# Kernel tuning notes

Hardware: AMD Instinct MI355X
Metric: run time of the kernel (lower is better)

Reference implementation:

```python
import jax, jax.numpy as jnp
import numpy as np

B, T, D_MODEL, HEAD_SIZE = 8, 1024, 1024, 64
BLOCK_SIZE = 1024  # == max_relative_pos


def setup_inputs() -> dict:
    key = jax.random.key(0)
    ks = jax.random.split(key, 7)
    s = 1.0 / np.sqrt(D_MODEL)
    return {
        "x": jax.random.normal(ks[0], (B, T, D_MODEL), dtype=jnp.float32),
        "Wk": jax.random.normal(ks[1], (D_MODEL, HEAD_SIZE), dtype=jnp.float32) * s,
        "bk": jax.random.normal(ks[2], (HEAD_SIZE,), dtype=jnp.float32) * 0.02,
        "Wq": jax.random.normal(ks[3], (D_MODEL, HEAD_SIZE), dtype=jnp.float32) * s,
        "bq": jax.random.normal(ks[4], (HEAD_SIZE,), dtype=jnp.float32) * 0.02,
        "Wv": jax.random.normal(ks[5], (D_MODEL, HEAD_SIZE), dtype=jnp.float32) * s,
        "rel_emb": jax.random.normal(ks[6], (2 * BLOCK_SIZE + 1, HEAD_SIZE), dtype=jnp.float32) * 0.02,
        "mask": 1,
    }


def reference(x, Wk, bk, Wq, bq, Wv, rel_emb, mask):
    Bb, Tt, _ = x.shape
    hs = Wk.shape[1]
    max_rel = (rel_emb.shape[0] - 1) // 2

    k = x @ Wk + bk          # [B,T,hs]
    q = x @ Wq + bq          # [B,T,hs]
    v = x @ Wv               # [B,T,hs]

    pos = jnp.arange(Tt)
    idx = jnp.clip(pos[:, None] - pos[None, :], -max_rel, max_rel) + max_rel
    r = rel_emb[idx]         # [T,T,hs], r[i,j] = emb(clip(i-j))

    # scores[b,i,j] = (q[b,i] + r[i,j]) . (k[b,j] + r[j,i]) / sqrt(hs)
    scale = 1.0 / np.sqrt(hs).astype(np.float32)
    scores = (
        jnp.einsum("bid,bjd->bij", q, k)
        + jnp.einsum("bid,jid->bij", q, r)   # q_i . r[j,i]
        + jnp.einsum("ijd,bjd->bij", r, k)   # r[i,j] . k_j
        + jnp.einsum("ijd,jid->ij", r, r)[None]  # r[i,j] . r[j,i]
    ) * scale

    if mask:  # static Python int -> causal mask, matches tril masked_fill
        causal = jnp.tril(jnp.ones((Tt, Tt), dtype=bool))
        scores = jnp.where(causal, scores, jnp.float32(-jnp.inf))

    w = jax.nn.softmax(scores, axis=-1)  # dropout is identity in eval mode
    return w @ v  # [B,T,hs]
```

## Files before the change

kernel.cpp:

```cpp
#include <hip/hip_runtime.h>
#include <hip/hip_bf16.h>
#include <math.h>


typedef __hip_bfloat16 bf16;
typedef __attribute__((ext_vector_type(8))) short short8;
typedef __attribute__((ext_vector_type(4))) float f32x4;

#define NTILE32 528
#define MFMA16(a, b, c) __builtin_amdgcn_mfma_f32_16x16x32_bf16(a, b, c, 0, 0, 0)

__device__ __forceinline__ float bf2f(bf16 h) { return __bfloat162float(h); }
__device__ __forceinline__ bf16 f2bf(float f) { return __float2bfloat16(f); }
__device__ __forceinline__ short bfs(float f) {
  bf16 h = __float2bfloat16(f);
  return *(short*)&h;
}

union U16 {
  uint4 u;
  short8 s;
};
__device__ __forceinline__ short8 ldfrag(const bf16* p) {
  U16 x;
  x.u = *(const uint4*)p;
  return x.s;
}

__global__ __launch_bounds__(256) void prep_kernel(
    const float* __restrict__ Wk, const float* __restrict__ Wq, const float* __restrict__ Wv,
    const float* __restrict__ E, bf16* __restrict__ WT, bf16* __restrict__ Ep,
    bf16* __restrict__ Erev, float* __restrict__ rrG, float* __restrict__ zeroBase) {
  const int bid = blockIdx.x, t = threadIdx.x;
  if (bid < 768) {
    int idx = bid * 256 + t;
    int sel = idx >> 16, r = idx & 65535;
    int n = r >> 10, kk = r & 1023;
    const float* W = (sel == 0) ? Wk : (sel == 1) ? Wq : Wv;
    WT[idx] = f2bf(W[kk * 64 + n]);
  } else if (bid < 1281) {
    int idx = (bid - 768) * 256 + t;
    if (idx < 2049 * 64) {
      int tt = idx >> 6, d = idx & 63;
      Ep[idx] = f2bf(E[idx]);
      Erev[idx] = f2bf(E[(size_t)(2048 - tt) * 64 + d]);
    }
  } else if (bid < 1537) {
    int dlt = ((bid - 1281) << 2) + (t >> 6);
    int d = t & 63;
    float p = E[(size_t)(1024 + dlt) * 64 + d] * E[(size_t)(1024 - dlt) * 64 + d];
#pragma unroll
    for (int off = 32; off > 0; off >>= 1) p += __shfl_down(p, off);
    if (d == 0) rrG[64 + dlt] = p;
  } else {
    int idx4 = (bid - 1537) * 256 + t;
    if (idx4 * 4 < 532480)
      *(float4*)(zeroBase + idx4 * 4) = make_float4(0.f, 0.f, 0.f, 0.f);
  }
}

__global__ __launch_bounds__(256, 2) void qkv_mfma(
    const float* __restrict__ x, const bf16* __restrict__ WT,
    const float* __restrict__ bk, const float* __restrict__ bq,
    bf16* __restrict__ qB, bf16* __restrict__ kB, bf16* __restrict__ vT) {
  const int R0 = blockIdx.x << 4;
  const int t = threadIdx.x;
  const int lane = t & 63, wave = t >> 6;
  const int m = lane & 15, quad = lane >> 4;

  __shared__ float RED[4][16][196];
  __shared__ bf16 VTS[64][24];

  const float* xrow = x + (size_t)(R0 + m) * 1024 + (wave << 8);
  f32x4 acc[3][4];
#pragma unroll
  for (int s = 0; s < 3; ++s)
#pragma unroll
    for (int c = 0; c < 4; ++c) acc[s][c] = (f32x4){0.f, 0.f, 0.f, 0.f};

#pragma unroll
  for (int ks = 0; ks < 8; ++ks) {
    const int k0 = ks * 32 + quad * 8;
    float4 xa = *(const float4*)(xrow + k0);
    float4 xb = *(const float4*)(xrow + k0 + 4);
    short8 a;
    a[0] = bfs(xa.x); a[1] = bfs(xa.y); a[2] = bfs(xa.z); a[3] = bfs(xa.w);
    a[4] = bfs(xb.x); a[5] = bfs(xb.y); a[6] = bfs(xb.z); a[7] = bfs(xb.w);
    const int kg = (wave << 8) + k0;
#pragma unroll
    for (int sel = 0; sel < 3; ++sel)
#pragma unroll
      for (int ct = 0; ct < 4; ++ct) {
        const bf16* bb = WT + ((size_t)(sel * 64 + ct * 16 + m) << 10) + kg;
        acc[sel][ct] = MFMA16(a, ldfrag(bb), acc[sel][ct]);
      }
  }

#pragma unroll
  for (int sel = 0; sel < 3; ++sel)
#pragma unroll
    for (int ct = 0; ct < 4; ++ct)
#pragma unroll
      for (int r = 0; r < 4; ++r)
        RED[wave][quad * 4 + r][sel * 64 + ct * 16 + m] = acc[sel][ct][r];
  __syncthreads();

#pragma unroll
  for (int e = 0; e < 12; ++e) {
    int idx = e * 256 + t;
    int row = idx / 192, c = idx - row * 192;
    float s = RED[0][row][c] + RED[1][row][c] + RED[2][row][c] + RED[3][row][c];
    int sel = c >> 6, col = c & 63;
    size_t grow = (size_t)(R0 + row);
    if (sel == 0) kB[grow * 64 + col] = f2bf(s + bk[col]);
    else if (sel == 1) qB[grow * 64 + col] = f2bf(s + bq[col]);
    else VTS[col][row] = f2bf(s);
  }
  __syncthreads();
  {
    int dd = t >> 2, h = (t & 3) << 2;
    int b = R0 >> 10, tloc = R0 & 1023;
    *(uint2*)(vT + ((size_t)((b << 6) + dd) << 10) + tloc + h) = *(const uint2*)&VTS[dd][h];
  }
}

__global__ __launch_bounds__(256, 4) void flash_mfma(
    const bf16* __restrict__ qB, const bf16* __restrict__ kB, const bf16* __restrict__ vT,
    const bf16* __restrict__ Ep, const bf16* __restrict__ Erev, const float* __restrict__ rrG,
    float* __restrict__ Oacc, float* __restrict__ Lacc) {
  const int t = threadIdx.x;
  const int lane = t & 63, wave = t >> 6;
  const int m = lane & 15, quad = lane >> 4;

  const int g = (blockIdx.x << 2) + wave;
  const int b = g / NTILE32;
  const int r0 = g - b * NTILE32;
  int it = (int)((sqrtf(8.f * r0 + 1.f) - 1.f) * 0.5f);
  while ((it + 1) * (it + 2) / 2 <= r0) ++it;
  while (it * (it + 1) / 2 > r0) --it;
  const int jt = r0 - it * (it + 1) / 2;
  const int I0 = it << 5, J0 = jt << 5;
  const int D = I0 - J0, w0 = D - 32;

  __shared__ __align__(16) bf16 M2S[4][32][68];
  __shared__ __align__(16) bf16 M3S[4][32][68];
  bf16 (*M2)[68] = M2S[wave];
  bf16 (*M3)[68] = M3S[wave];
  bf16 (*PS)[40] = (bf16(*)[40]) & M3S[wave][0][0];

  const bf16* qb = qB + ((size_t)((b << 10) + I0) << 6);
  const bf16* kb = kB + ((size_t)((b << 10) + J0) << 6);
  short8 aq[2][2], kf[2][2];
#pragma unroll
  for (int rt = 0; rt < 2; ++rt)
#pragma unroll
    for (int ks = 0; ks < 2; ++ks) {
      aq[rt][ks] = ldfrag(qb + ((rt * 16 + m) << 6) + ks * 32 + quad * 8);
      kf[rt][ks] = ldfrag(kb + ((rt * 16 + m) << 6) + ks * 32 + quad * 8);
    }

  const bf16* erb = Erev + ((size_t)(1024 + w0) << 6);
  const bf16* epb = Ep + ((size_t)(1024 + w0) << 6);
#pragma unroll
  for (int ct = 0; ct < 4; ++ct) {
    const bf16* b2p = erb + ((size_t)(ct * 16 + m) << 6) + quad * 8;
    const bf16* b3p = epb + ((size_t)(ct * 16 + m) << 6) + quad * 8;
    const short8 b20 = ldfrag(b2p);
    const short8 b21 = ldfrag(b2p + 32);
    const short8 b30 = ldfrag(b3p);
    const short8 b31 = ldfrag(b3p + 32);
    const float rv = rrG[64 + w0 + ct * 16 + m];
#pragma unroll
    for (int rt = 0; rt < 2; ++rt) {
      f32x4 c2 = (f32x4){0.f, 0.f, 0.f, 0.f};
      c2 = MFMA16(aq[rt][0], b20, c2);
      c2 = MFMA16(aq[rt][1], b21, c2);
      f32x4 c3 = (f32x4){0.f, 0.f, 0.f, 0.f};
      c3 = MFMA16(kf[rt][0], b30, c3);
      c3 = MFMA16(kf[rt][1], b31, c3);
#pragma unroll
      for (int r = 0; r < 4; ++r) {
        M2[rt * 16 + quad * 4 + r][ct * 16 + m] = f2bf(c2[r] + rv);
        M3[rt * 16 + quad * 4 + r][ct * 16 + m] = f2bf(c3[r]);
      }
    }
  }

  f32x4 acc[2][2];
#pragma unroll
  for (int rt = 0; rt < 2; ++rt)
#pragma unroll
    for (int ct = 0; ct < 2; ++ct) {
      f32x4 c = (f32x4){0.f, 0.f, 0.f, 0.f};
      c = MFMA16(aq[rt][0], kf[ct][0], c);
      c = MFMA16(aq[rt][1], kf[ct][1], c);
      acc[rt][ct] = c;
    }

  float sc[2][2][4], lr[2][4];
#pragma unroll
  for (int rt = 0; rt < 2; ++rt)
#pragma unroll
    for (int r = 0; r < 4; ++r) lr[rt][r] = 0.f;
#pragma unroll
  for (int ct = 0; ct < 2; ++ct) {
    const int uj = ct * 16 + m;
#pragma unroll
    for (int rt = 0; rt < 2; ++rt)
#pragma unroll
      for (int r = 0; r < 4; ++r) {
        const int ui = rt * 16 + quad * 4 + r;
        float p = 0.f;
        if (ui - uj + D >= 0) {
          const int wi = ui - uj + 32;
          const float sv = (acc[rt][ct][r] + bf2f(M2[ui][wi]) + bf2f(M3[uj][wi])) * 0.125f;
          p = __expf(sv - 8.0f);
        }
        sc[ct][rt][r] = p;
        lr[rt][r] += p;
      }
  }
#pragma unroll
  for (int rt = 0; rt < 2; ++rt)
#pragma unroll
    for (int r = 0; r < 4; ++r) {
#pragma unroll
      for (int off = 1; off < 16; off <<= 1) lr[rt][r] += __shfl_xor(lr[rt][r], off);
    }
  if (m == 0) {
#pragma unroll
    for (int rt = 0; rt < 2; ++rt)
#pragma unroll
      for (int r = 0; r < 4; ++r)
        atomicAdd(&Lacc[(b << 10) + I0 + rt * 16 + quad * 4 + r], lr[rt][r]);
  }

#pragma unroll
  for (int ct = 0; ct < 2; ++ct)
#pragma unroll
    for (int rt = 0; rt < 2; ++rt)
#pragma unroll
      for (int r = 0; r < 4; ++r)
        PS[rt * 16 + quad * 4 + r][ct * 16 + m] = f2bf(sc[ct][rt][r]);

  short8 ap[2];
#pragma unroll
  for (int rt = 0; rt < 2; ++rt) ap[rt] = ldfrag(&PS[rt * 16 + m][quad * 8]);
  float* ob = Oacc + ((size_t)((b << 10) + I0) << 6);
#pragma unroll
  for (int ct = 0; ct < 4; ++ct) {
    const short8 vf = ldfrag(vT + ((size_t)(b * 64 + ct * 16 + m) << 10) + J0 + quad * 8);
#pragma unroll
    for (int rt = 0; rt < 2; ++rt) {
      f32x4 o = (f32x4){0.f, 0.f, 0.f, 0.f};
      o = MFMA16(ap[rt], vf, o);
#pragma unroll
      for (int r = 0; r < 4; ++r)
        atomicAdd(&ob[(size_t)(rt * 16 + quad * 4 + r) * 64 + ct * 16 + m], o[r]);
    }
  }
}

__global__ __launch_bounds__(256) void normalize_kernel(
    const float* __restrict__ Oacc, const float* __restrict__ Lacc, float* __restrict__ out) {
  int idx = blockIdx.x * 256 + threadIdx.x;
  out[idx] = Oacc[idx] / Lacc[idx >> 6];
}

extern "C" void kernel_launch(void* const* d_in, const int* in_sizes, int n_in,
                              void* d_out, int out_size, void* d_ws, size_t ws_size,
                              hipStream_t stream) {
  const float* x = (const float*)d_in[0];
  const float* Wk = (const float*)d_in[1];
  const float* bk = (const float*)d_in[2];
  const float* Wq = (const float*)d_in[3];
  const float* bq = (const float*)d_in[4];
  const float* Wv = (const float*)d_in[5];
  const float* E = (const float*)d_in[6];
  float* out = (float*)d_out;

  float* wsf = (float*)d_ws;
  float* Oacc = wsf;
  float* Lacc = wsf + 524288;
  float* rrG = wsf + 532480;
  bf16* qB = (bf16*)(rrG + 1152);
  bf16* kB = qB + 524288;
  bf16* vT = kB + 524288;
  bf16* Ep = vT + 524288;
  bf16* Erev = Ep + 131200;
  bf16* WT = Erev + 131200;

  prep_kernel<<<2058, 256, 0, stream>>>(Wk, Wq, Wv, E, WT, Ep, Erev, rrG, Oacc);
  qkv_mfma<<<512, 256, 0, stream>>>(x, WT, bk, bq, qB, kB, vT);
  flash_mfma<<<1056, 256, 0, stream>>>(qB, kB, vT, Ep, Erev, rrG, Oacc, Lacc);
  normalize_kernel<<<2048, 256, 0, stream>>>(Oacc, Lacc, out);
}
```

Before: 157.7 us.

## Replace atomic output accumulation with per-tile partial buffers reduced in normalize

Each 32x32 tile of the attention kernel now writes its P@V partial output to its own slot in a large workspace with plain stores, where it previously did float atomicAdds into a shared accumulator. The normalize kernel then sums the partials for each row tile across the causal column tiles before dividing by the softmax denominator. This removes atomic contention and the need to zero the output accumulator, so the prep kernel only clears Lacc. The cost is much more memory traffic: roughly 8.6M floats written and then read back, about 34 MB, instead of 0.5M atomics.

```diff
diff --git a/kernel.cpp b/kernel.cpp
--- a/kernel.cpp
+++ b/kernel.cpp
@@ -54,7 +54,7 @@
     if (d == 0) rrG[64 + dlt] = p;
   } else {
     int idx4 = (bid - 1537) * 256 + t;
-    if (idx4 * 4 < 532480)
+    if (idx4 < 2048)
       *(float4*)(zeroBase + idx4 * 4) = make_float4(0.f, 0.f, 0.f, 0.f);
   }
 }
@@ -127,7 +127,7 @@
 __global__ __launch_bounds__(256, 4) void flash_mfma(
     const bf16* __restrict__ qB, const bf16* __restrict__ kB, const bf16* __restrict__ vT,
     const bf16* __restrict__ Ep, const bf16* __restrict__ Erev, const float* __restrict__ rrG,
-    float* __restrict__ Oacc, float* __restrict__ Lacc) {
+    float* __restrict__ Opart, float* __restrict__ Lacc) {
   const int t = threadIdx.x;
   const int lane = t & 63, wave = t >> 6;
   const int m = lane & 15, quad = lane >> 4;
@@ -246,7 +246,7 @@
   short8 ap[2];
 #pragma unroll
   for (int rt = 0; rt < 2; ++rt) ap[rt] = ldfrag(&PS[rt * 16 + m][quad * 8]);
-  float* ob = Oacc + ((size_t)((b << 10) + I0) << 6);
+  float* obp = Opart + ((size_t)(b * NTILE32 + r0) << 11);
 #pragma unroll
   for (int ct = 0; ct < 4; ++ct) {
     const short8 vf = ldfrag(vT + ((size_t)(b * 64 + ct * 16 + m) << 10) + J0 + quad * 8);
@@ -256,15 +256,28 @@
       o = MFMA16(ap[rt], vf, o);
 #pragma unroll
       for (int r = 0; r < 4; ++r)
-        atomicAdd(&ob[(size_t)(rt * 16 + quad * 4 + r) * 64 + ct * 16 + m], o[r]);
+        obp[(size_t)((rt * 16 + quad * 4 + r) * 64 + ct * 16 + m)] = o[r];
     }
   }
 }
 
 __global__ __launch_bounds__(256) void normalize_kernel(
-    const float* __restrict__ Oacc, const float* __restrict__ Lacc, float* __restrict__ out) {
-  int idx = blockIdx.x * 256 + threadIdx.x;
-  out[idx] = Oacc[idx] / Lacc[idx >> 6];
+    const float* __restrict__ Opart, const float* __restrict__ Lacc, float* __restrict__ out) {
+  const int idx = blockIdx.x * 256 + threadIdx.x;
+  const int b = idx >> 16;
+  const int rem = idx & 65535;
+  const int i = rem >> 6, d = rem & 63;
+  const int it = i >> 5;
+  const int base = (it * (it + 1)) >> 1;
+  const float* sp = Opart + ((size_t)(b * NTILE32 + base) << 11) + ((i & 31) << 6) + d;
+  float s0 = 0.f, s1 = 0.f;
+  int jt = 0;
+  for (; jt + 1 <= it; jt += 2) {
+    s0 += sp[(size_t)jt << 11];
+    s1 += sp[(size_t)(jt + 1) << 11];
+  }
+  if (jt <= it) s0 += sp[(size_t)jt << 11];
+  out[idx] = (s0 + s1) / Lacc[idx >> 6];
 }
 
 extern "C" void kernel_launch(void* const* d_in, const int* in_sizes, int n_in,
@@ -280,9 +293,9 @@
   float* out = (float*)d_out;
 
   float* wsf = (float*)d_ws;
-  float* Oacc = wsf;
-  float* Lacc = wsf + 524288;
-  float* rrG = wsf + 532480;
+  float* Opart = wsf;
+  float* Lacc = wsf + 8650752;
+  float* rrG = Lacc + 8192;
   bf16* qB = (bf16*)(rrG + 1152);
   bf16* kB = qB + 524288;
   bf16* vT = kB + 524288;
@@ -290,8 +303,8 @@
   bf16* Erev = Ep + 131200;
   bf16* WT = Erev + 131200;
 
-  prep_kernel<<<2058, 256, 0, stream>>>(Wk, Wq, Wv, E, WT, Ep, Erev, rrG, Oacc);
+  prep_kernel<<<1545, 256, 0, stream>>>(Wk, Wq, Wv, E, WT, Ep, Erev, rrG, Lacc);
   qkv_mfma<<<512, 256, 0, stream>>>(x, WT, bk, bq, qB, kB, vT);
-  flash_mfma<<<1056, 256, 0, stream>>>(qB, kB, vT, Ep, Erev, rrG, Oacc, Lacc);
-  normalize_kernel<<<2048, 256, 0, stream>>>(Oacc, Lacc, out);
-}
+  flash_mfma<<<1056, 256, 0, stream>>>(qB, kB, vT, Ep, Erev, rrG, Opart, Lacc);
+  normalize_kernel<<<2048, 256, 0, stream>>>(Opart, Lacc, out);
+}
```

Measured after the change: 144.5 us. -8.4%, faster.
